# Kernel optimization log

Hardware: AMD Instinct MI355X
Metric: run time of the kernel (lower is better)

Reference implementation:

```python
import jax, jax.numpy as jnp
import numpy as np

K = 16
EPS = 1e-5


def _bn_relu(x, gamma, beta):
    # BatchNorm1d in training mode (biased batch stats over edge dim) + ReLU
    mu = jnp.mean(x, axis=0)
    var = jnp.mean((x - mu) ** 2, axis=0)
    xh = (x - mu) * jax.lax.rsqrt(var + EPS)
    return jax.nn.relu(xh * gamma + beta)


def setup_inputs() -> dict:
    key = jax.random.key(0)
    ks = jax.random.split(key, 8)
    N, F, H = 16384, 64, 128
    s_in = 1.0 / np.sqrt(2 * F)
    s_h = 1.0 / np.sqrt(H)
    return {
        "X": jax.random.normal(ks[0], (N, F), dtype=jnp.float32),
        "W1": jax.random.uniform(ks[1], (2 * F, H), jnp.float32, -s_in, s_in),
        "b1": jnp.zeros((H,), jnp.float32),
        "g1": jnp.ones((H,), jnp.float32),
        "beta1": jnp.zeros((H,), jnp.float32),
        "W2": jax.random.uniform(ks[2], (H, H), jnp.float32, -s_h, s_h),
        "b2": jnp.zeros((H,), jnp.float32),
        "g2": jnp.ones((H,), jnp.float32),
        "beta2": jnp.zeros((H,), jnp.float32),
        "W3": jax.random.uniform(ks[3], (H, H), jnp.float32, -s_h, s_h),
        "b3": jnp.zeros((H,), jnp.float32),
        "g3": jnp.ones((H,), jnp.float32),
        "beta3": jnp.zeros((H,), jnp.float32),
    }


def reference(X, W1, b1, g1, beta1, W2, b2, g2, beta2, W3, b3, g3, beta3):
    N, F = X.shape
    # --- dynamic kNN graph (includes self, matching torch_cluster.knn(x, x, k)) ---
    n2 = jnp.sum(X * X, axis=1)                       # [N]
    D = n2[:, None] + n2[None, :] - 2.0 * (X @ X.T)   # [N, N] squared dists
    _, idx = jax.lax.top_k(-D, K)                     # [N, K] neighbor indices
    # --- edge feature gather: [x_i, x_j - x_i] ---
    xj = X[idx]                                       # [N, K, F]
    xi = jnp.broadcast_to(X[:, None, :], (N, K, F))
    e = jnp.concatenate([xi, xj - xi], axis=-1).reshape(N * K, 2 * F)
    # --- edge MLP: (Linear -> BN -> ReLU) x 3 ---
    h = _bn_relu(e @ W1 + b1, g1, beta1)
    h = _bn_relu(h @ W2 + b2, g2, beta2)
    h = _bn_relu(h @ W3 + b3, g3, beta3)
    # --- scatter aggregate (aggr='add'): sum over the K neighbors of each node ---
    return h.reshape(N, K, -1).sum(axis=1)            # [N, H]
```

## Files before the change

kernel.cpp:

```cpp
#include <hip/hip_runtime.h>


#define N_PTS 16384
#define FDIM  64
#define HDIM  128
#define KNN   16
#define NEDGE (N_PTS * KNN)

#define SENT_KEY 0xFF800000FFFFFFFFull
#define MAXU64   0xFFFFFFFFFFFFFFFFull
#define EPS_MARGIN 1.0f

typedef __attribute__((ext_vector_type(8)))  short bf16x8;
typedef __attribute__((ext_vector_type(16))) float f32x16;

__global__ __launch_bounds__(256)
void k_norms(const float* __restrict__ X, float* __restrict__ n2) {
  const int r = blockIdx.x * 256 + threadIdx.x;
  const float4* x4 = reinterpret_cast<const float4*>(X) + (size_t)r * (FDIM / 4);
  float p[16];
#pragma unroll
  for (int i = 0; i < 16; ++i) {
    const float4 v = x4[i];
    p[i] = (v.x * v.x + v.y * v.y) + (v.z * v.z + v.w * v.w);
  }
#pragma unroll
  for (int s = 1; s < 16; s <<= 1) {
#pragma unroll
    for (int i = 0; i < 16; i += 2 * s) p[i] += p[i + s];
  }
  n2[r] = p[0];
}

__global__ __launch_bounds__(256)
void k_split(const float* __restrict__ X, unsigned short* __restrict__ Xh,
             unsigned short* __restrict__ Xl) {
  const int t = blockIdx.x * 256 + threadIdx.x;
  const float4* X4 = reinterpret_cast<const float4*>(X);
  const float4 v0 = X4[(size_t)t * 2];
  const float4 v1 = X4[(size_t)t * 2 + 1];
  const float xs[8] = {v0.x, v0.y, v0.z, v0.w, v1.x, v1.y, v1.z, v1.w};
  unsigned int h[8], l[8];
#pragma unroll
  for (int e = 0; e < 8; ++e) {
    const unsigned int u = __float_as_uint(xs[e]);
    h[e] = (u + 0x7FFFu + ((u >> 16) & 1u)) >> 16;
    const float hf = __uint_as_float(h[e] << 16);
    const float r = xs[e] - hf;
    const unsigned int v = __float_as_uint(r);
    l[e] = (v + 0x7FFFu + ((v >> 16) & 1u)) >> 16;
  }
  uint4 hw, lw;
  hw.x = h[0] | (h[1] << 16); hw.y = h[2] | (h[3] << 16);
  hw.z = h[4] | (h[5] << 16); hw.w = h[6] | (h[7] << 16);
  lw.x = l[0] | (l[1] << 16); lw.y = l[2] | (l[3] << 16);
  lw.z = l[4] | (l[5] << 16); lw.w = l[6] | (l[7] << 16);
  reinterpret_cast<uint4*>(Xh)[t] = hw;
  reinterpret_cast<uint4*>(Xl)[t] = lw;
}

__global__ __launch_bounds__(256)
void k_pq(const float* __restrict__ X, const float* __restrict__ W1,
          const float* __restrict__ b1, float* __restrict__ P, float* __restrict__ Q) {
  const int h4 = threadIdx.x & 31;
  const int rsub = threadIdx.x >> 5;
  const int row = blockIdx.x * 8 + rsub;
  const float* x = X + (size_t)row * FDIM;
  const float4* W14 = reinterpret_cast<const float4*>(W1);
  float4 at = make_float4(0.f, 0.f, 0.f, 0.f);
  float4 ab = make_float4(0.f, 0.f, 0.f, 0.f);
#pragma unroll 8
  for (int f = 0; f < FDIM; ++f) {
    const float xv = x[f];
    const float4 wt = W14[(size_t)f * 32 + h4];
    const float4 wb = W14[(size_t)(FDIM + f) * 32 + h4];
    at.x = fmaf(xv, wt.x, at.x); at.y = fmaf(xv, wt.y, at.y);
    at.z = fmaf(xv, wt.z, at.z); at.w = fmaf(xv, wt.w, at.w);
    ab.x = fmaf(xv, wb.x, ab.x); ab.y = fmaf(xv, wb.y, ab.y);
    ab.z = fmaf(xv, wb.z, ab.z); ab.w = fmaf(xv, wb.w, ab.w);
  }
  const float4 bb = reinterpret_cast<const float4*>(b1)[h4];
  float4 pv;
  pv.x = at.x - ab.x + bb.x; pv.y = at.y - ab.y + bb.y;
  pv.z = at.z - ab.z + bb.z; pv.w = at.w - ab.w + bb.w;
  reinterpret_cast<float4*>(P)[(size_t)row * 32 + h4] = pv;
  reinterpret_cast<float4*>(Q)[(size_t)row * 32 + h4] = ab;
}

__global__ __launch_bounds__(256, 2)
void k_dist_mfma(const float* __restrict__ X, const unsigned short* __restrict__ Xh,
                 const unsigned short* __restrict__ Xl, const float* __restrict__ n2g,
                 int* __restrict__ knn) {
  __shared__ __align__(16) char smem[32768];
  float* Xi = reinterpret_cast<float*>(smem);
  float* thr = reinterpret_cast<float*>(smem + 8192);
  unsigned int* ring = reinterpret_cast<unsigned int*>(smem + 9216);

  const int tid = threadIdx.x;
  const int w = tid >> 6, lane = tid & 63;
  const int li = lane & 31, hf = lane >> 5;
  const int i0 = blockIdx.x * 32;
  const int slot = w * 2 + hf;

  const float4* X4 = reinterpret_cast<const float4*>(X);

  thr[tid] = __int_as_float(0x7f800000);
  for (int u = tid; u < 512; u += 256) {
    const int row = u >> 4, c4 = u & 15;
    const float4 v = X4[(size_t)(i0 + row) * 16 + c4];
    *reinterpret_cast<float4*>(&Xi[row * 64 + ((c4 ^ (row & 15)) * 4)]) = v;
  }

  bf16x8 bh[4], bl[4];
#pragma unroll
  for (int s = 0; s < 4; ++s) {
    const size_t o = (size_t)(i0 + li) * 64 + s * 16 + hf * 8;
    bh[s] = *reinterpret_cast<const bf16x8*>(Xh + o);
    bl[s] = *reinterpret_cast<const bf16x8*>(Xl + o);
  }
  const float n2i = n2g[i0 + li];

  unsigned long long list[16];
#pragma unroll
  for (int p = 0; p < 16; ++p) list[p] = SENT_KEY;
  int cnt = 0;
  float thrm = __int_as_float(0x7f800000);

  __syncthreads();

  auto flush = [&]() {
#pragma unroll 1
    for (int s = 0; s < 6; ++s) {
      if (s < cnt) {
        const unsigned int j = ring[s * 256 + tid];
        float a = 0.0f;
        const float4* xj4 = reinterpret_cast<const float4*>(X + (size_t)j * 64);
#pragma unroll
        for (int c4 = 0; c4 < 16; ++c4) {
          const float4 xiv =
              *reinterpret_cast<const float4*>(&Xi[li * 64 + ((c4 ^ (li & 15)) * 4)]);
          const float4 xjv = xj4[c4];
          a = fmaf(xiv.x, xjv.x, a); a = fmaf(xiv.y, xjv.y, a);
          a = fmaf(xiv.z, xjv.z, a); a = fmaf(xiv.w, xjv.w, a);
        }
        const float t = n2i + n2g[j];
        const float sd = __fsub_rn(t, __fmul_rn(2.0f, a));
        unsigned int ub = __float_as_uint(sd);
        ub = (ub & 0x80000000u) ? ~ub : (ub | 0x80000000u);
        const unsigned long long key = ((unsigned long long)ub << 32) | j;
        if (key < list[15]) {
#pragma unroll
          for (int q = 15; q >= 1; --q) {
            const unsigned long long prev = list[q - 1];
            unsigned long long cur = list[q];
            cur = (key < cur) ? key : cur;
            list[q] = (key < prev) ? prev : cur;
          }
          list[0] = (key < list[0]) ? key : list[0];
        }
      }
    }
    cnt = 0;
    const unsigned int ub16 = (unsigned int)(list[15] >> 32);
    const float tf = (ub16 & 0x80000000u) ? __uint_as_float(ub16 & 0x7fffffffu)
                                          : __uint_as_float(~ub16);
    thr[slot * 32 + li] = tf;
    thrm = fminf(thrm, tf);
  };

  for (int ct = 0; ct < 128; ++ct) {
    const int jb = (ct * 4 + w) * 32;
    if ((ct & 3) == 0) {
      float m = thr[li];
#pragma unroll
      for (int q = 1; q < 8; ++q) m = fminf(m, thr[q * 32 + li]);
      thrm = m;
    }
    bf16x8 ah[4], al[4];
#pragma unroll
    for (int s = 0; s < 4; ++s) {
      const size_t o = (size_t)(jb + li) * 64 + s * 16 + hf * 8;
      ah[s] = *reinterpret_cast<const bf16x8*>(Xh + o);
      al[s] = *reinterpret_cast<const bf16x8*>(Xl + o);
    }
    float4 nj[4];
#pragma unroll
    for (int q = 0; q < 4; ++q)
      nj[q] = *reinterpret_cast<const float4*>(n2g + jb + q * 8 + hf * 4);

    f32x16 acc0 = {0,0,0,0,0,0,0,0,0,0,0,0,0,0,0,0};
    f32x16 acc1 = {0,0,0,0,0,0,0,0,0,0,0,0,0,0,0,0};
#pragma unroll
    for (int s = 0; s < 4; ++s) {
      acc0 = __builtin_amdgcn_mfma_f32_32x32x16_bf16(ah[s], bh[s], acc0, 0, 0, 0);
      acc1 = __builtin_amdgcn_mfma_f32_32x32x16_bf16(ah[s], bl[s], acc1, 0, 0, 0);
      acc1 = __builtin_amdgcn_mfma_f32_32x32x16_bf16(al[s], bh[s], acc1, 0, 0, 0);
    }

    const float lim = thrm + EPS_MARGIN;
#pragma unroll
    for (int r = 0; r < 16; ++r) {
      const float dot = acc0[r] + acc1[r];
      const float njv = (r & 2) ? ((r & 1) ? nj[r >> 2].w : nj[r >> 2].z)
                                : ((r & 1) ? nj[r >> 2].y : nj[r >> 2].x);
      const float sv = fmaf(-2.0f, dot, n2i + njv);
      if (sv <= lim) {
        ring[cnt * 256 + tid] = (unsigned int)(jb + (r & 3) + 8 * (r >> 2) + 4 * hf);
        ++cnt;
      }
      if ((r & 1) && __any(cnt >= 5)) flush();
    }
  }
  flush();

  __syncthreads();
  unsigned long long* mb = reinterpret_cast<unsigned long long*>(smem);
#pragma unroll
  for (int p = 0; p < 16; ++p) mb[((size_t)li * 8 + slot) * 16 + p] = list[p];
  __syncthreads();
  if (tid < 32) {
    int pp[8] = {0, 0, 0, 0, 0, 0, 0, 0};
    for (int pick = 0; pick < KNN; ++pick) {
      unsigned long long best = MAXU64; int bq = 0;
#pragma unroll
      for (int q = 0; q < 8; ++q) {
        const unsigned long long cand =
            (pp[q] < 16) ? mb[((size_t)tid * 8 + q) * 16 + pp[q]] : MAXU64;
        if (cand < best) { best = cand; bq = q; }
      }
      pp[bq]++;
      knn[(size_t)(i0 + tid) * KNN + pick] = (int)(unsigned int)(best & 0xFFFFFFFFULL);
    }
  }
}

__global__ __launch_bounds__(256)
void k_stats_edges(const float* __restrict__ P, const float* __restrict__ Q,
                   const int* __restrict__ idx,
                   double* __restrict__ psum, double* __restrict__ psq) {
  __shared__ double sd[2][128];
  __shared__ double qd[2][128];
  const int t = threadIdx.x;
  const int h = t & 127, half = t >> 7;
  const size_t e0 = (size_t)blockIdx.x * 128;
  double s = 0.0, q = 0.0;
  for (int it = 0; it < 64; ++it) {
    const size_t e = e0 + (size_t)it * 2 + half;
    const int n = (int)(e >> 4);
    const int j = idx[e];
    const float v = P[(size_t)n * HDIM + h] + Q[(size_t)j * HDIM + h];
    s += (double)v;
    q += (double)v * (double)v;
  }
  sd[half][h] = s; qd[half][h] = q;
  __syncthreads();
  if (t < 128) {
    psum[(size_t)blockIdx.x * 128 + t] = sd[0][t] + sd[1][t];
    psq[(size_t)blockIdx.x * 128 + t]  = qd[0][t] + qd[1][t];
  }
}

__global__ __launch_bounds__(256)
void k_reduce_stats(const double* __restrict__ psum, const double* __restrict__ psq,
                    const float* __restrict__ g, const float* __restrict__ beta,
                    float* __restrict__ aout, float* __restrict__ cout) {
  __shared__ double sbuf[256];
  __shared__ double qbuf[256];
  const int h = blockIdx.x, t = threadIdx.x;
  double s = 0.0, q = 0.0;
  for (int i = t; i < 2048; i += 256) {
    s += psum[(size_t)i * 128 + h];
    q += psq[(size_t)i * 128 + h];
  }
  sbuf[t] = s; qbuf[t] = q;
  __syncthreads();
  for (int st = 128; st > 0; st >>= 1) {
    if (t < st) { sbuf[t] += sbuf[t + st]; qbuf[t] += qbuf[t + st]; }
    __syncthreads();
  }
  if (t == 0) {
    const double cntd = (double)NEDGE;
    const double mu = sbuf[0] / cntd;
    double var = qbuf[0] / cntd - mu * mu;
    if (var < 0.0) var = 0.0;
    const double rs = 1.0 / sqrt(var + 1e-5);
    const double a = (double)g[h] * rs;
    aout[h] = (float)a;
    cout[h] = (float)((double)beta[h] - mu * a);
  }
}

template <int MODE>
__global__ __launch_bounds__(256, 2)
void k_gemm(const float* __restrict__ P, const float* __restrict__ Q,
            const int* __restrict__ idx, float* __restrict__ big,
            const float* __restrict__ Wg, const float* __restrict__ bias,
            const float* __restrict__ aff_a, const float* __restrict__ aff_c,
            double* __restrict__ psum, double* __restrict__ psq) {
  __shared__ float A_lds[32][132];
  __shared__ float B_lds[32][132];
  const int tid = threadIdx.x;
  const int tm = tid & 15, tn = tid >> 4;
  const size_t e0 = (size_t)blockIdx.x * 128;

  float acc[2][2][4][4] = {};

  for (int kk = 0; kk < 128; kk += 32) {
    __syncthreads();
    {
      const int k4 = tid & 7;
      const int mrow = tid >> 3;
      const float4 av = reinterpret_cast<const float4*>(aff_a)[(kk >> 2) + k4];
      const float4 cv = reinterpret_cast<const float4*>(aff_c)[(kk >> 2) + k4];
#pragma unroll
      for (int p = 0; p < 4; ++p) {
        const int m = p * 32 + mrow;
        const size_t e = e0 + m;
        float4 hv;
        if (MODE == 2) {
          const int n = (int)(e >> 4);
          const int j = idx[e];
          const float4 pv = reinterpret_cast<const float4*>(P)[(size_t)n * 32 + (kk >> 2) + k4];
          const float4 qv = reinterpret_cast<const float4*>(Q)[(size_t)j * 32 + (kk >> 2) + k4];
          hv.x = pv.x + qv.x; hv.y = pv.y + qv.y; hv.z = pv.z + qv.z; hv.w = pv.w + qv.w;
        } else {
          hv = reinterpret_cast<const float4*>(big)[e * 32 + (kk >> 2) + k4];
        }
        A_lds[k4 * 4 + 0][m] = fmaxf(fmaf(av.x, hv.x, cv.x), 0.0f);
        A_lds[k4 * 4 + 1][m] = fmaxf(fmaf(av.y, hv.y, cv.y), 0.0f);
        A_lds[k4 * 4 + 2][m] = fmaxf(fmaf(av.z, hv.z, cv.z), 0.0f);
        A_lds[k4 * 4 + 3][m] = fmaxf(fmaf(av.w, hv.w, cv.w), 0.0f);
      }
    }
    {
      const int f4c = tid & 31;
      const int rb = tid >> 5;
#pragma unroll
      for (int p = 0; p < 4; ++p) {
        const int r = p * 8 + rb;
        const float4 wv = reinterpret_cast<const float4*>(Wg)[(size_t)(kk + r) * 32 + f4c];
        *reinterpret_cast<float4*>(&B_lds[r][f4c * 4]) = wv;
      }
    }
    __syncthreads();
#pragma unroll 4
    for (int k = 0; k < 32; ++k) {
      const float4 a0 = *reinterpret_cast<const float4*>(&A_lds[k][tm * 4]);
      const float4 a1 = *reinterpret_cast<const float4*>(&A_lds[k][64 + tm * 4]);
      const float4 b0 = *reinterpret_cast<const float4*>(&B_lds[k][tn * 4]);
      const float4 b1 = *reinterpret_cast<const float4*>(&B_lds[k][64 + tn * 4]);
      const float avv[2][4] = {{a0.x, a0.y, a0.z, a0.w}, {a1.x, a1.y, a1.z, a1.w}};
      const float bvv[2][4] = {{b0.x, b0.y, b0.z, b0.w}, {b1.x, b1.y, b1.z, b1.w}};
#pragma unroll
      for (int rh = 0; rh < 2; ++rh)
#pragma unroll
        for (int a = 0; a < 4; ++a)
#pragma unroll
          for (int ch = 0; ch < 2; ++ch)
#pragma unroll
            for (int b = 0; b < 4; ++b)
              acc[rh][ch][a][b] = fmaf(avv[rh][a], bvv[ch][b], acc[rh][ch][a][b]);
    }
  }

  __syncthreads();
  float sumf[2][4] = {{0, 0, 0, 0}, {0, 0, 0, 0}};
  float sqf[2][4]  = {{0, 0, 0, 0}, {0, 0, 0, 0}};
  const float4 bbl = reinterpret_cast<const float4*>(bias)[tn];
  const float4 bbh = reinterpret_cast<const float4*>(bias)[16 + tn];
  const float bb[2][4] = {{bbl.x, bbl.y, bbl.z, bbl.w}, {bbh.x, bbh.y, bbh.z, bbh.w}};
#pragma unroll
  for (int rh = 0; rh < 2; ++rh) {
#pragma unroll
    for (int a = 0; a < 4; ++a) {
      const size_t e = e0 + rh * 64 + tm * 4 + a;
#pragma unroll
      for (int ch = 0; ch < 2; ++ch) {
        float v[4];
#pragma unroll
        for (int b = 0; b < 4; ++b) {
          v[b] = acc[rh][ch][a][b] + bb[ch][b];
          sumf[ch][b] += v[b];
          sqf[ch][b] = fmaf(v[b], v[b], sqf[ch][b]);
        }
        float4 vv; vv.x = v[0]; vv.y = v[1]; vv.z = v[2]; vv.w = v[3];
        reinterpret_cast<float4*>(big)[e * 32 + ch * 16 + tn] = vv;
      }
    }
  }
  float* sds = reinterpret_cast<float*>(&A_lds[0][0]);
  float* sdq = reinterpret_cast<float*>(&B_lds[0][0]);
#pragma unroll
  for (int ch = 0; ch < 2; ++ch)
#pragma unroll
    for (int b = 0; b < 4; ++b) {
      sds[tm * 128 + ch * 64 + tn * 4 + b] = sumf[ch][b];
      sdq[tm * 128 + ch * 64 + tn * 4 + b] = sqf[ch][b];
    }
  __syncthreads();
  if (tid < 128) {
    double s = 0.0, q = 0.0;
#pragma unroll
    for (int m2 = 0; m2 < 16; ++m2) {
      s += (double)sds[m2 * 128 + tid];
      q += (double)sdq[m2 * 128 + tid];
    }
    psum[(size_t)blockIdx.x * 128 + tid] = s;
    psq[(size_t)blockIdx.x * 128 + tid]  = q;
  }
}

__global__ __launch_bounds__(256)
void k_final(const float* __restrict__ big, const float* __restrict__ a3,
             const float* __restrict__ c3, float* __restrict__ out) {
  const int t = threadIdx.x;
  const int h = t & 127, ns = t >> 7;
  const size_t n = (size_t)blockIdx.x * 2 + ns;
  const float aa = a3[h], cc = c3[h];
  float s = 0.0f;
#pragma unroll
  for (int k = 0; k < KNN; ++k) {
    const float x = big[(n * KNN + k) * HDIM + h];
    s += fmaxf(fmaf(aa, x, cc), 0.0f);
  }
  out[n * HDIM + h] = s;
}

extern "C" void kernel_launch(void* const* d_in, const int* in_sizes, int n_in,
                              void* d_out, int out_size, void* d_ws, size_t ws_size,
                              hipStream_t stream) {
  (void)in_sizes; (void)n_in; (void)out_size;
  const float* X   = (const float*)d_in[0];
  const float* W1  = (const float*)d_in[1];
  const float* b1  = (const float*)d_in[2];
  const float* g1  = (const float*)d_in[3];
  const float* be1 = (const float*)d_in[4];
  const float* W2  = (const float*)d_in[5];
  const float* b2  = (const float*)d_in[6];
  const float* g2  = (const float*)d_in[7];
  const float* be2 = (const float*)d_in[8];
  const float* W3  = (const float*)d_in[9];
  const float* b3  = (const float*)d_in[10];
  const float* g3  = (const float*)d_in[11];
  const float* be3 = (const float*)d_in[12];
  float* out = (float*)d_out;

  char* w = (char*)d_ws;
  size_t off = 0;
  auto carve = [&](size_t bytes) -> char* {
    char* p = w + off;
    off = (off + bytes + 255) & ~(size_t)255;
    return p;
  };
  float*  n2   = (float*)carve((size_t)N_PTS * 4);
  unsigned short* Xh = (unsigned short*)carve((size_t)N_PTS * FDIM * 2);
  unsigned short* Xl = (unsigned short*)carve((size_t)N_PTS * FDIM * 2);
  float*  P    = (float*)carve((size_t)N_PTS * HDIM * 4);
  float*  Q    = (float*)carve((size_t)N_PTS * HDIM * 4);
  int*    knn  = (int*)carve((size_t)NEDGE * 4);
  double* ps1  = (double*)carve((size_t)2048 * 128 * 8);
  double* pq1  = (double*)carve((size_t)2048 * 128 * 8);
  double* ps2  = (double*)carve((size_t)2048 * 128 * 8);
  double* pq2  = (double*)carve((size_t)2048 * 128 * 8);
  double* ps3  = (double*)carve((size_t)2048 * 128 * 8);
  double* pq3  = (double*)carve((size_t)2048 * 128 * 8);
  float*  a1   = (float*)carve(512);
  float*  c1   = (float*)carve(512);
  float*  a2   = (float*)carve(512);
  float*  c2   = (float*)carve(512);
  float*  a3   = (float*)carve(512);
  float*  c3   = (float*)carve(512);
  float*  big  = (float*)carve((size_t)NEDGE * HDIM * 4);
  if (off > ws_size) return;

  k_norms<<<dim3(N_PTS / 256), dim3(256), 0, stream>>>(X, n2);
  k_split<<<dim3(512), dim3(256), 0, stream>>>(X, Xh, Xl);
  k_pq<<<dim3(N_PTS / 8), dim3(256), 0, stream>>>(X, W1, b1, P, Q);
  k_dist_mfma<<<dim3(N_PTS / 32), dim3(256), 0, stream>>>(X, Xh, Xl, n2, knn);
  k_stats_edges<<<dim3(2048), dim3(256), 0, stream>>>(P, Q, knn, ps1, pq1);
  k_reduce_stats<<<dim3(128), dim3(256), 0, stream>>>(ps1, pq1, g1, be1, a1, c1);
  k_gemm<2><<<dim3(NEDGE / 128), dim3(256), 0, stream>>>(P, Q, knn, big, W2, b2, a1, c1, ps2, pq2);
  k_reduce_stats<<<dim3(128), dim3(256), 0, stream>>>(ps2, pq2, g2, be2, a2, c2);
  k_gemm<3><<<dim3(NEDGE / 128), dim3(256), 0, stream>>>(P, Q, knn, big, W3, b3, a2, c2, ps3, pq3);
  k_reduce_stats<<<dim3(128), dim3(256), 0, stream>>>(ps3, pq3, g3, be3, a3, c3);
  k_final<<<dim3(N_PTS / 2), dim3(256), 0, stream>>>(big, a3, c3, out);
}
```

Before: 1.088 ms.

## Split kNN candidate range across two blocks per query tile and merge

The distance/top-k kernel now launches two blocks per 32-query tile, each scanning half of the candidate points and writing a sorted partial top-16 list of packed keys. A new merge kernel combines the two sorted lists into the final neighbor indices. The aim is to double the grid size for better CU occupancy and load balance, since 512 blocks may underfill the GPU. In exchange it adds a partial buffer, an extra launch, and weaker pruning thresholds, because each half starts its filtering from scratch.

```diff
diff --git a/kernel.cpp b/kernel.cpp
--- a/kernel.cpp
+++ b/kernel.cpp
@@ -90,7 +90,7 @@
 __global__ __launch_bounds__(256, 2)
 void k_dist_mfma(const float* __restrict__ X, const unsigned short* __restrict__ Xh,
                  const unsigned short* __restrict__ Xl, const float* __restrict__ n2g,
-                 int* __restrict__ knn) {
+                 unsigned long long* __restrict__ part) {
   __shared__ __align__(16) char smem[32768];
   float* Xi = reinterpret_cast<float*>(smem);
   float* thr = reinterpret_cast<float*>(smem + 8192);
@@ -99,7 +99,10 @@
   const int tid = threadIdx.x;
   const int w = tid >> 6, lane = tid & 63;
   const int li = lane & 31, hf = lane >> 5;
-  const int i0 = blockIdx.x * 32;
+  const int it = blockIdx.x >> 1;
+  const int half = blockIdx.x & 1;
+  const int i0 = it * 32;
+  const int j0 = half * 8192;
   const int slot = w * 2 + hf;
 
   const float4* X4 = reinterpret_cast<const float4*>(X);
@@ -168,8 +171,8 @@
     thrm = fminf(thrm, tf);
   };
 
-  for (int ct = 0; ct < 128; ++ct) {
-    const int jb = (ct * 4 + w) * 32;
+  for (int ct = 0; ct < 64; ++ct) {
+    const int jb = j0 + (ct * 4 + w) * 32;
     if ((ct & 3) == 0) {
       float m = thr[li];
 #pragma unroll
@@ -220,6 +223,7 @@
   __syncthreads();
   if (tid < 32) {
     int pp[8] = {0, 0, 0, 0, 0, 0, 0, 0};
+    unsigned long long* dst = part + ((size_t)(i0 + tid) * 2 + half) * 16;
     for (int pick = 0; pick < KNN; ++pick) {
       unsigned long long best = MAXU64; int bq = 0;
 #pragma unroll
@@ -229,8 +233,25 @@
         if (cand < best) { best = cand; bq = q; }
       }
       pp[bq]++;
-      knn[(size_t)(i0 + tid) * KNN + pick] = (int)(unsigned int)(best & 0xFFFFFFFFULL);
-    }
+      dst[pick] = best;
+    }
+  }
+}
+
+__global__ __launch_bounds__(256)
+void k_merge2(const unsigned long long* __restrict__ part, int* __restrict__ knn) {
+  const int i = blockIdx.x * 256 + threadIdx.x;
+  const unsigned long long* a = part + (size_t)i * 32;
+  const unsigned long long* b = a + 16;
+  int pa = 0, pb = 0;
+#pragma unroll
+  for (int k = 0; k < KNN; ++k) {
+    const unsigned long long va = a[pa];
+    const unsigned long long vb = b[pb];
+    const bool ta = (va <= vb);
+    knn[(size_t)i * KNN + k] = (int)(unsigned int)((ta ? va : vb) & 0xFFFFFFFFULL);
+    pa += ta ? 1 : 0;
+    pb += ta ? 0 : 1;
   }
 }
 
@@ -458,6 +479,7 @@
   float*  P    = (float*)carve((size_t)N_PTS * HDIM * 4);
   float*  Q    = (float*)carve((size_t)N_PTS * HDIM * 4);
   int*    knn  = (int*)carve((size_t)NEDGE * 4);
+  unsigned long long* part = (unsigned long long*)carve((size_t)N_PTS * 32 * 8);
   double* ps1  = (double*)carve((size_t)2048 * 128 * 8);
   double* pq1  = (double*)carve((size_t)2048 * 128 * 8);
   double* ps2  = (double*)carve((size_t)2048 * 128 * 8);
@@ -476,7 +498,8 @@
   k_norms<<<dim3(N_PTS / 256), dim3(256), 0, stream>>>(X, n2);
   k_split<<<dim3(512), dim3(256), 0, stream>>>(X, Xh, Xl);
   k_pq<<<dim3(N_PTS / 8), dim3(256), 0, stream>>>(X, W1, b1, P, Q);
-  k_dist_mfma<<<dim3(N_PTS / 32), dim3(256), 0, stream>>>(X, Xh, Xl, n2, knn);
+  k_dist_mfma<<<dim3(N_PTS / 32 * 2), dim3(256), 0, stream>>>(X, Xh, Xl, n2, part);
+  k_merge2<<<dim3(N_PTS / 256), dim3(256), 0, stream>>>(part, knn);
   k_stats_edges<<<dim3(2048), dim3(256), 0, stream>>>(P, Q, knn, ps1, pq1);
   k_reduce_stats<<<dim3(128), dim3(256), 0, stream>>>(ps1, pq1, g1, be1, a1, c1);
   k_gemm<2><<<dim3(NEDGE / 128), dim3(256), 0, stream>>>(P, Q, knn, big, W2, b2, a1, c1, ps2, pq2);
```

After: 1.476 ms. 1.36x slower.
